# Kernel tuning notes

Measured on AMD Instinct MI355X. Metric: run time of the kernel, lower is better.

## Reference

```python
import jax, jax.numpy as jnp
import numpy as np

N = 50000
E = 800000
IN, HID, OUT = 256, 128, 128
H = 2


def gat_conv(x, edge_src, edge_dst, W, att_src, att_dst, bias, concat=True):
    # PyG GATConv: x' = W x, edge attention e = leaky_relu(a_s.x'_src + a_d.x'_dst),
    # softmax over incoming edges of each dst node, weighted scatter-add.
    n = x.shape[0]
    heads, ch = att_src.shape
    xl = (x @ W).reshape(n, heads, ch)                      # [N,H,C]
    a_src = jnp.sum(xl * att_src[None], axis=-1)            # [N,H]
    a_dst = jnp.sum(xl * att_dst[None], axis=-1)            # [N,H]
    e = a_src[edge_src] + a_dst[edge_dst]                   # [E,H]
    e = jax.nn.leaky_relu(e, negative_slope=0.2)
    # segment softmax over dst neighborhoods (self-loops guarantee non-empty)
    emax = jax.ops.segment_max(e, edge_dst, num_segments=n)
    ee = jnp.exp(e - emax[edge_dst])
    denom = jax.ops.segment_sum(ee, edge_dst, num_segments=n)
    alpha = ee / (denom[edge_dst] + 1e-16)                  # [E,H]
    msg = xl[edge_src] * alpha[:, :, None]                  # [E,H,C]
    out = jax.ops.segment_sum(msg, edge_dst, num_segments=n)  # [N,H,C]
    out = out.reshape(n, heads * ch) if concat else out.mean(axis=1)
    return out + bias


def setup_inputs() -> dict:
    key = jax.random.key(0)
    ks = jax.random.split(key, 12)
    x = jax.random.normal(ks[0], (N, IN), dtype=jnp.float32)
    edge_index = jax.random.randint(ks[1], (2, E), 0, N, dtype=jnp.int64)
    node_type = (jnp.arange(N, dtype=jnp.int64) % 3)
    agent_idx = jnp.arange(0, N, 3, dtype=jnp.int64)  # nodes with type 0
    # layer 0: in=256 -> out=128, heads=2, concat
    W0 = jax.random.normal(ks[2], (IN, H * HID), dtype=jnp.float32) / np.sqrt(IN)
    as0 = jax.random.normal(ks[3], (H, HID), dtype=jnp.float32) / np.sqrt(HID)
    ad0 = jax.random.normal(ks[4], (H, HID), dtype=jnp.float32) / np.sqrt(HID)
    b0 = jnp.zeros((H * HID,), dtype=jnp.float32)
    # layer 1: in=128*2 -> out=128, heads=2, concat (average_last=False)
    W1 = jax.random.normal(ks[5], (H * HID, H * OUT), dtype=jnp.float32) / np.sqrt(H * HID)
    as1 = jax.random.normal(ks[6], (H, OUT), dtype=jnp.float32) / np.sqrt(OUT)
    ad1 = jax.random.normal(ks[7], (H, OUT), dtype=jnp.float32) / np.sqrt(OUT)
    b1 = jnp.zeros((H * OUT,), dtype=jnp.float32)
    return {"x": x, "edge_index": edge_index, "node_type": node_type,
            "agent_idx": agent_idx, "W0": W0, "as0": as0, "ad0": ad0, "b0": b0,
            "W1": W1, "as1": as1, "ad1": ad1, "b1": b1}


def reference(x, edge_index, node_type, agent_idx, W0, as0, ad0, b0, W1, as1, ad1, b1):
    # add self loops (PyG GATConv default add_self_loops=True)
    loop = jnp.arange(N, dtype=edge_index.dtype)
    src = jnp.concatenate([edge_index[0], loop])
    dst = jnp.concatenate([edge_index[1], loop])
    final = []
    h = gat_conv(x, src, dst, W0, as0, ad0, b0, concat=True)
    h = jax.nn.sigmoid(h)
    final.append(h[agent_idx])  # full_receptive_field=True
    h = gat_conv(h, src, dst, W1, as1, ad1, b1, concat=True)
    h = jax.nn.sigmoid(h)
    final.append(h[agent_idx])
    return jnp.concatenate(final, axis=1)  # [n_agents, 128*2 + 128*2]
```

## Files before the change

kernel.cpp:

```cpp
#include <hip/hip_runtime.h>
#include <hip/hip_fp16.h>

typedef unsigned short u16;
typedef unsigned int   u32;
typedef unsigned char  u8;
typedef __attribute__((ext_vector_type(8))) short short8;
typedef __attribute__((ext_vector_type(8))) unsigned short ushort8v;
typedef __attribute__((ext_vector_type(4))) float f32x4;

#define TPB 256

#define GLDS16(g,l) __builtin_amdgcn_global_load_lds( \
    (const __attribute__((address_space(1))) void*)(g), \
    (__attribute__((address_space(3))) void*)(l), 16, 0, 0)

__device__ __forceinline__ float b2f(u16 u){ u32 x=((u32)u)<<16; return __uint_as_float(x); }
__device__ __forceinline__ u16 f2b(float f){ u32 x=__float_as_uint(f); u32 r=x+0x7FFFu+((x>>16)&1u); return (u16)(r>>16); }
__device__ __forceinline__ float lrelu(float x){ return x>0.f?x:0.2f*x; }
__device__ __forceinline__ float sigm(float x){ return 1.f/(1.f+__expf(-x)); }

__device__ __forceinline__ float4 ld4(const void* p, size_t i4, int isbf){
  if(isbf){
    ushort4 u=((const ushort4*)p)[i4];
    return make_float4(b2f(u.x),b2f(u.y),b2f(u.z),b2f(u.w));
  }
  return ((const float4*)p)[i4];
}
__device__ __forceinline__ float ld1(const void* p, size_t i, int isbf){
  return isbf ? b2f(((const u16*)p)[i]) : ((const float*)p)[i];
}

__global__ void k_detect(const u16* __restrict__ w, int* __restrict__ flag){
  __shared__ int s[256];
  int t=threadIdx.x, sane=0;
  for(int i=t;i<512;i+=256){
    u16 u=w[i]; u32 e=(u>>7)&0xFFu;
    if((e>=103u&&e<=143u)||((u&0x7FFFu)==0u)) sane++;
  }
  s[t]=sane; __syncthreads();
  for(int o=128;o;o>>=1){ if(t<o) s[t]+=s[t+o]; __syncthreads(); }
  if(t==0) flag[0]=(s[0]>=480)?1:0;
}

__global__ __launch_bounds__(256) void k_x8(const void* __restrict__ X, u16* __restrict__ xb,
                                            int n8, const int* __restrict__ flag){
  int i=blockIdx.x*256+threadIdx.x; if(i>=n8) return;
  size_t e=(size_t)i*8;
  if(flag[0]){
    *(ushort8v*)(xb+e)=*(const ushort8v*)((const u16*)X+e);
  }else{
    const float4* fp=(const float4*)((const float*)X+e);
    float4 f0=fp[0], f1=fp[1];
    ushort8v o;
    o[0]=f2b(f0.x); o[1]=f2b(f0.y); o[2]=f2b(f0.z); o[3]=f2b(f0.w);
    o[4]=f2b(f1.x); o[5]=f2b(f1.y); o[6]=f2b(f1.z); o[7]=f2b(f1.w);
    *(ushort8v*)(xb+e)=o;
  }
}

__global__ void k_deg(const int* __restrict__ dst, int E, int N, int* __restrict__ deg){
  int e=blockIdx.x*blockDim.x+threadIdx.x; if(e>=E+N) return;
  int d=(e<E)?dst[e]:(e-E);
  d=min(max(d,0),N-1);
  atomicAdd(&deg[d],1);
}

__global__ void k_scan(const int* __restrict__ deg, int* __restrict__ rs,
                       int* __restrict__ counter, int n,
                       const int* __restrict__ aidx, int* __restrict__ ainv, int na){
  __shared__ int tmp[TPB];
  __shared__ int base;
  int i=blockIdx.x*TPB+threadIdx.x;
  if(i<na){ int a=aidx[i]; if(a>=0&&a<n) ainv[a]=i; }
  int v=(i<n)?deg[i]:0;
  tmp[threadIdx.x]=v; __syncthreads();
  for(int off=1;off<TPB;off<<=1){
    int t=(threadIdx.x>=off)?tmp[threadIdx.x-off]:0;
    __syncthreads();
    tmp[threadIdx.x]+=t;
    __syncthreads();
  }
  if(threadIdx.x==TPB-1) base=atomicAdd(counter,tmp[TPB-1]);
  __syncthreads();
  if(i<n) rs[i]=base+tmp[threadIdx.x]-v;
}

__global__ void k_fill(const int* __restrict__ src, const int* __restrict__ dst, int E, int N,
                       const int* __restrict__ rs, int* __restrict__ fill, int* __restrict__ col){
  int e=blockIdx.x*blockDim.x+threadIdx.x; if(e>=E+N) return;
  int d,s;
  if(e<E){ d=dst[e]; s=src[e]; } else { d=e-E; s=e-E; }
  d=min(max(d,0),N-1); s=min(max(s,0),N-1);
  int p=rs[d]+atomicAdd(&fill[d],1);
  col[p]=s;
}

__global__ __launch_bounds__(256) void k_trans(const void* __restrict__ Wa, u16* __restrict__ WTa,
                                               const void* __restrict__ Wb, u16* __restrict__ WTb,
                                               const int* __restrict__ flag){
  __shared__ float s[64][65];
  const void* W = blockIdx.z ? Wb : Wa;
  u16* WT = blockIdx.z ? WTb : WTa;
  const int isbf=flag[0];
  int tx=threadIdx.x&63, ty=threadIdx.x>>6;
  int k0=blockIdx.x*64, n0=blockIdx.y*64;
  #pragma unroll
  for(int i=0;i<64;i+=4)
    s[ty+i][tx]=ld1(W,(size_t)(k0+ty+i)*256+n0+tx,isbf);
  __syncthreads();
  #pragma unroll
  for(int i=0;i<64;i+=4)
    WT[(size_t)(n0+ty+i)*256+k0+tx]=f2b(s[tx][ty+i]);
}

__global__ __launch_bounds__(256) void k_gemm(const u16* __restrict__ A, const u16* __restrict__ BT,
                                              u16* __restrict__ C, int M){
  __shared__ short As[128*32];
  __shared__ short Bs[128*32];
  const int t=threadIdx.x;
  const int lane=t&63, wv=t>>6;
  const int wm=wv>>1, wn=wv&1;
  const int m15=lane&15, kg=lane>>4;
  const int gm0=blockIdx.x*128, n0=blockIdx.y*128;
  int r0=wv*32+(lane>>2), r1=r0+16;
  int slot=lane&3;
  int kq0=slot^((r0>>1)&3), kq1=slot^((r1>>1)&3);
  int ga0=gm0+r0; ga0=ga0<M?ga0:M-1;
  int ga1=gm0+r1; ga1=ga1<M?ga1:M-1;
  const u16* ap0=A+(size_t)ga0*256+kq0*8;
  const u16* ap1=A+(size_t)ga1*256+kq1*8;
  const u16* bp0=BT+(size_t)(n0+r0)*256+kq0*8;
  const u16* bp1=BT+(size_t)(n0+r1)*256+kq1*8;
  short* al0=As+(wv*32)*32;
  short* al1=As+(wv*32+16)*32;
  short* bl0=Bs+(wv*32)*32;
  short* bl1=Bs+(wv*32+16)*32;
  f32x4 acc[4][4]={};
  for(int k0=0;k0<256;k0+=32){
    GLDS16(ap0+k0,al0); GLDS16(ap1+k0,al1);
    GLDS16(bp0+k0,bl0); GLDS16(bp1+k0,bl1);
    __syncthreads();
    short8 af[4], bf[4];
    #pragma unroll
    for(int mi=0;mi<4;++mi){
      int row=wm*64+mi*16+m15;
      af[mi]=*(const short8*)&As[row*32+((kg^((row>>1)&3)))*8];
    }
    #pragma unroll
    for(int ni=0;ni<4;++ni){
      int row=wn*64+ni*16+m15;
      bf[ni]=*(const short8*)&Bs[row*32+((kg^((row>>1)&3)))*8];
    }
    #pragma unroll
    for(int mi=0;mi<4;++mi)
      #pragma unroll
      for(int ni=0;ni<4;++ni)
        acc[mi][ni]=__builtin_amdgcn_mfma_f32_16x16x32_bf16(af[mi],bf[ni],acc[mi][ni],0,0,0);
    __syncthreads();
  }
  #pragma unroll
  for(int mi=0;mi<4;++mi){
    #pragma unroll
    for(int r=0;r<4;++r){
      int grow=gm0+wm*64+mi*16+kg*4+r;
      if(grow<M){
        #pragma unroll
        for(int ni=0;ni<4;++ni){
          int gcol=n0+wn*64+ni*16+m15;
          C[(size_t)grow*256+gcol]=f2b(acc[mi][ni][r]);
        }
      }
    }
  }
}

__global__ __launch_bounds__(256) void k_att(const u16* __restrict__ xl, const void* __restrict__ as_,
                                             const void* __restrict__ ad_, float4* __restrict__ asv,
                                             float2* __restrict__ adv, u8* __restrict__ xl8,
                                             int n, const int* __restrict__ flag){
  const int isbf=flag[0];
  int w=(blockIdx.x*256+threadIdx.x)>>6;
  int lane=threadIdx.x&63;
  if(w>=n) return;
  int ch=lane*4;
  ushort4 u=*(const ushort4*)(xl+(size_t)w*256+ch);
  float4 s=ld4(as_,ch>>2,isbf);
  float4 d=ld4(ad_,ch>>2,isbf);
  float x0=b2f(u.x),x1=b2f(u.y),x2=b2f(u.z),x3=b2f(u.w);
  float m=fmaxf(fmaxf(fabsf(x0),fabsf(x1)),fmaxf(fabsf(x2),fabsf(x3)));
  for(int off=32;off;off>>=1) m=fmaxf(m,__shfl_xor(m,off));
  float mm=fmaxf(m,1e-20f);
  float scale=mm*(1.f/127.f);
  float rsc=127.f/mm;
  int q0=(int)rintf(fmaf(x0,rsc,128.f));
  int q1=(int)rintf(fmaf(x1,rsc,128.f));
  int q2=(int)rintf(fmaf(x2,rsc,128.f));
  int q3=(int)rintf(fmaf(x3,rsc,128.f));
  u32 pack=(u32)q0|((u32)q1<<8)|((u32)q2<<16)|((u32)q3<<24);
  ((u32*)(xl8+(size_t)w*256))[lane]=pack;
  float ps=x0*s.x+x1*s.y+x2*s.z+x3*s.w;
  float pd=x0*d.x+x1*d.y+x2*d.z+x3*d.w;
  for(int off=16;off;off>>=1){ ps+=__shfl_xor(ps,off); pd+=__shfl_xor(pd,off); }
  float ps1=__shfl(ps,32), pd1=__shfl(pd,32);
  if(lane==0){
    asv[w]=make_float4(ps,ps1,scale,0.f);
    adv[w]=make_float2(pd,pd1);
  }
}

__global__ __launch_bounds__(256) void k_alpha(const int* __restrict__ rs, const int* __restrict__ deg,
    const int* __restrict__ col, const float4* __restrict__ asv, const float2* __restrict__ adv,
    int2* __restrict__ ew, float2* __restrict__ rden, int n){
  int w=(blockIdx.x*256+threadIdx.x)>>6;
  int lane=threadIdx.x&63;
  if(w>=n) return;
  int s0=rs[w], cnt=deg[w];
  float2 ad=adv[w];
  float sum0=0.f, sum1=0.f;
  for(int base=0;base<cnt;base+=64){
    int j=base+lane;
    if(j<cnt){
      int sv=col[s0+j];
      float4 a=asv[sv];
      float e0=fminf(lrelu(a.x+ad.x),11.f);
      float e1=fminf(lrelu(a.y+ad.y),11.f);
      float w0=__expf(e0), w1=__expf(e1);
      sum0+=w0; sum1+=w1;
      __half2 p=__floats2half2_rn(w0*a.z,w1*a.z);
      ew[s0+j]=make_int2(sv,*(int*)&p);
    }
  }
  for(int off=32;off;off>>=1){ sum0+=__shfl_xor(sum0,off); sum1+=__shfl_xor(sum1,off); }
  if(lane==0) rden[w]=make_float2(1.f/(sum0+1e-16f),1.f/(sum1+1e-16f));
}

__global__ __launch_bounds__(256) void k_agg(const int* __restrict__ rs, const int* __restrict__ deg,
    const int2* __restrict__ ew, const float2* __restrict__ rden,
    const u8* __restrict__ xl8, const void* __restrict__ bias,
    u16* __restrict__ hout, void* __restrict__ out, int ostride, int ocol,
    const int* __restrict__ ainv, int n, const int* __restrict__ flag){
  const int isbf=flag[0];
  int w=(blockIdx.x*blockDim.x+threadIdx.x)>>5;
  int sl=threadIdx.x&31;
  if(w>=n) return;
  int s0=rs[w], cnt=deg[w];
  int ch=sl*8, h=sl>>4;
  float acc[8]={};
  float sumw=0.f;
  for(int j=0;j<cnt;j+=4){
    int2 e[4];
    #pragma unroll
    for(int u=0;u<4;++u){
      int idx=j+u; idx=idx<cnt?idx:cnt-1;
      e[u]=ew[s0+idx];
    }
    uint2 rv[4];
    #pragma unroll
    for(int u=0;u<4;++u)
      rv[u]=*(const uint2*)(xl8+(size_t)e[u].x*256+ch);
    #pragma unroll
    for(int u=0;u<4;++u){
      __half2 p=*(__half2*)&e[u].y;
      float wb=__half2float(h?__high2half(p):__low2half(p));
      wb=(j+u<cnt)?wb:0.f;
      u32 a=rv[u].x, b=rv[u].y;
      acc[0]=fmaf(wb,(float)( a     &255u),acc[0]);
      acc[1]=fmaf(wb,(float)((a>> 8)&255u),acc[1]);
      acc[2]=fmaf(wb,(float)((a>>16)&255u),acc[2]);
      acc[3]=fmaf(wb,(float)( a>>24      ),acc[3]);
      acc[4]=fmaf(wb,(float)( b     &255u),acc[4]);
      acc[5]=fmaf(wb,(float)((b>> 8)&255u),acc[5]);
      acc[6]=fmaf(wb,(float)((b>>16)&255u),acc[6]);
      acc[7]=fmaf(wb,(float)( b>>24      ),acc[7]);
      sumw+=wb;
    }
  }
  float2 rd=rden[w];
  float rh=h?rd.y:rd.x;
  float4 b0=ld4(bias,ch>>2,isbf);
  float4 b1=ld4(bias,(ch>>2)+1,isbf);
  float c=128.f*sumw;
  float r[8];
  r[0]=sigm((acc[0]-c)*rh+b0.x); r[1]=sigm((acc[1]-c)*rh+b0.y);
  r[2]=sigm((acc[2]-c)*rh+b0.z); r[3]=sigm((acc[3]-c)*rh+b0.w);
  r[4]=sigm((acc[4]-c)*rh+b1.x); r[5]=sigm((acc[5]-c)*rh+b1.y);
  r[6]=sigm((acc[6]-c)*rh+b1.z); r[7]=sigm((acc[7]-c)*rh+b1.w);
  ushort8v ov;
  #pragma unroll
  for(int q=0;q<8;++q) ov[q]=f2b(r[q]);
  if(hout) *(ushort8v*)(hout+(size_t)w*256+ch)=ov;
  int ar=ainv[w];
  if(ar>=0){
    size_t o=(size_t)ar*ostride+ocol+ch;
    if(isbf){
      *(ushort8v*)((u16*)out+o)=ov;
    }else{
      *(float4*)((float*)out+o)  =make_float4(r[0],r[1],r[2],r[3]);
      *(float4*)((float*)out+o+4)=make_float4(r[4],r[5],r[6],r[7]);
    }
  }
}

extern "C" void kernel_launch(void* const* d_in, const int* in_sizes, int n_in,
                              void* d_out, int out_size, void* d_ws, size_t ws_size,
                              hipStream_t stream) {
  const void* x   = d_in[0];
  const int*  ei  = (const int*)d_in[1];
  const int*  aidx= (const int*)d_in[3];
  const void* W0  = d_in[4];
  const void* as0 = d_in[5];
  const void* ad0 = d_in[6];
  const void* b0  = d_in[7];
  const void* W1  = d_in[8];
  const void* as1 = d_in[9];
  const void* ad1 = d_in[10];
  const void* b1  = d_in[11];

  const int N  = in_sizes[0]/256;
  const int E  = in_sizes[1]/2;
  const int na = in_sizes[3];
  const int Et = E+N;

  char* ws=(char*)d_ws; size_t off=0;
  auto alloc=[&](size_t bytes)->void*{ void* p=ws+off; off+=(bytes+255)&~(size_t)255; return p; };
  int*   flg =(int*) alloc(256);
  u16*   xl  =(u16*) alloc((size_t)N*256*2);
  u16*   h1  =(u16*) alloc((size_t)N*256*2);
  u8*    xl8 =(u8*)  alloc((size_t)N*256);
  u16*   WT0 =(u16*) alloc((size_t)256*256*2);
  u16*   WT1 =(u16*) alloc((size_t)256*256*2);
  float4* asv=(float4*)alloc((size_t)N*16);
  float2* adv=(float2*)alloc((size_t)N*8);
  char*  zbase=ws+off;
  int*   deg =(int*) alloc((size_t)N*4);
  int*   fill=(int*) alloc((size_t)N*4);
  int*   ctr =(int*) alloc(256);
  size_t zlen=(ws+off)-zbase;
  int*   rstp=(int*) alloc((size_t)N*4);
  int*   ainv=(int*) alloc((size_t)N*4);
  int*   col =(int*) alloc((size_t)Et*4);
  int2*  ew  =(int2*)alloc((size_t)Et*8);
  float2* rdn=(float2*)alloc((size_t)N*8);

  u16* xb = h1;

  const int* esrc=ei;
  const int* edst=ei+E;

  hipMemsetAsync(zbase,0,zlen,stream);
  hipMemsetAsync(ainv,0xFF,(size_t)N*4,stream);

  k_detect<<<1,256,0,stream>>>((const u16*)W0,flg);
  k_deg  <<<(Et+255)/256,256,0,stream>>>(edst,E,N,deg);
  k_scan <<<(N+TPB-1)/TPB,TPB,0,stream>>>(deg,rstp,ctr,N,aidx,ainv,na);
  k_fill <<<(Et+255)/256,256,0,stream>>>(esrc,edst,E,N,rstp,fill,col);
  k_trans<<<dim3(4,4,2),256,0,stream>>>(W0,WT0,W1,WT1,flg);
  k_x8   <<<(N*32+255)/256,256,0,stream>>>(x,xb,N*32,flg);

  dim3 gg((N+127)/128,2);
  k_gemm <<<gg,256,0,stream>>>(xb,WT0,xl,N);
  k_att  <<<(N+3)/4,256,0,stream>>>(xl,as0,ad0,asv,adv,xl8,N,flg);
  k_alpha<<<(N+3)/4,256,0,stream>>>(rstp,deg,col,asv,adv,ew,rdn,N);
  k_agg  <<<(N+7)/8,256,0,stream>>>(rstp,deg,ew,rdn,xl8,b0,h1,d_out,512,0,ainv,N,flg);
  k_gemm <<<gg,256,0,stream>>>(h1,WT1,xl,N);
  k_att  <<<(N+3)/4,256,0,stream>>>(xl,as1,ad1,asv,adv,xl8,N,flg);
  k_alpha<<<(N+3)/4,256,0,stream>>>(rstp,deg,col,asv,adv,ew,rdn,N);
  k_agg  <<<(N+7)/8,256,0,stream>>>(rstp,deg,ew,rdn,xl8,b1,(u16*)nullptr,d_out,512,256,ainv,N,flg);
}
```

Baseline: 386.0 us.

## Merge setup kernels, widen GEMM K-tile to 64, unroll aggregation by 8

Folds the dtype-detect kernel and the ainv memset into k_deg, and merges the weight transpose and input conversion into one k_prep launch, cutting launch count. The GEMM now stages 64-wide K tiles with an 8-way XOR swizzle, halving barrier iterations at the cost of more LDS. The aggregation loop gathers 8 neighbours per iteration instead of 4 to expose more memory-level parallelism, which raises register pressure. There is a possible race: k_deg block 0 writes the flag while other blocks run, but the flag is only read by later kernels, so this is fine.

```diff
diff --git a/kernel.cpp b/kernel.cpp
--- a/kernel.cpp
+++ b/kernel.cpp
@@ -30,37 +30,23 @@
   return isbf ? b2f(((const u16*)p)[i]) : ((const float*)p)[i];
 }
 
-__global__ void k_detect(const u16* __restrict__ w, int* __restrict__ flag){
-  __shared__ int s[256];
-  int t=threadIdx.x, sane=0;
-  for(int i=t;i<512;i+=256){
-    u16 u=w[i]; u32 e=(u>>7)&0xFFu;
-    if((e>=103u&&e<=143u)||((u&0x7FFFu)==0u)) sane++;
-  }
-  s[t]=sane; __syncthreads();
-  for(int o=128;o;o>>=1){ if(t<o) s[t]+=s[t+o]; __syncthreads(); }
-  if(t==0) flag[0]=(s[0]>=480)?1:0;
-}
-
-__global__ __launch_bounds__(256) void k_x8(const void* __restrict__ X, u16* __restrict__ xb,
-                                            int n8, const int* __restrict__ flag){
-  int i=blockIdx.x*256+threadIdx.x; if(i>=n8) return;
-  size_t e=(size_t)i*8;
-  if(flag[0]){
-    *(ushort8v*)(xb+e)=*(const ushort8v*)((const u16*)X+e);
-  }else{
-    const float4* fp=(const float4*)((const float*)X+e);
-    float4 f0=fp[0], f1=fp[1];
-    ushort8v o;
-    o[0]=f2b(f0.x); o[1]=f2b(f0.y); o[2]=f2b(f0.z); o[3]=f2b(f0.w);
-    o[4]=f2b(f1.x); o[5]=f2b(f1.y); o[6]=f2b(f1.z); o[7]=f2b(f1.w);
-    *(ushort8v*)(xb+e)=o;
-  }
-}
-
-__global__ void k_deg(const int* __restrict__ dst, int E, int N, int* __restrict__ deg){
-  int e=blockIdx.x*blockDim.x+threadIdx.x; if(e>=E+N) return;
-  int d=(e<E)?dst[e]:(e-E);
+__global__ void k_deg(const int* __restrict__ dst, int E, int N, int* __restrict__ deg,
+                      int* __restrict__ ainv, const u16* __restrict__ w0, int* __restrict__ flag){
+  int gid=blockIdx.x*blockDim.x+threadIdx.x;
+  if(blockIdx.x==0){
+    __shared__ int s[256];
+    int t=threadIdx.x, sane=0;
+    for(int i=t;i<512;i+=256){
+      u16 u=w0[i]; u32 e=(u>>7)&0xFFu;
+      if((e>=103u&&e<=143u)||((u&0x7FFFu)==0u)) sane++;
+    }
+    s[t]=sane; __syncthreads();
+    for(int o=128;o;o>>=1){ if(t<o) s[t]+=s[t+o]; __syncthreads(); }
+    if(t==0) flag[0]=(s[0]>=480)?1:0;
+  }
+  if(gid<N) ainv[gid]=-1;
+  if(gid>=E+N) return;
+  int d=(gid<E)?dst[gid]:(gid-E);
   d=min(max(d,0),N-1);
   atomicAdd(&deg[d],1);
 }
@@ -95,67 +81,84 @@
   col[p]=s;
 }
 
-__global__ __launch_bounds__(256) void k_trans(const void* __restrict__ Wa, u16* __restrict__ WTa,
-                                               const void* __restrict__ Wb, u16* __restrict__ WTb,
-                                               const int* __restrict__ flag){
-  __shared__ float s[64][65];
-  const void* W = blockIdx.z ? Wb : Wa;
-  u16* WT = blockIdx.z ? WTb : WTa;
+__global__ __launch_bounds__(256) void k_prep(const void* __restrict__ Wa, u16* __restrict__ WTa,
+                                              const void* __restrict__ Wb, u16* __restrict__ WTb,
+                                              const void* __restrict__ X, u16* __restrict__ xb,
+                                              int n8, const int* __restrict__ flag){
   const int isbf=flag[0];
-  int tx=threadIdx.x&63, ty=threadIdx.x>>6;
-  int k0=blockIdx.x*64, n0=blockIdx.y*64;
-  #pragma unroll
-  for(int i=0;i<64;i+=4)
-    s[ty+i][tx]=ld1(W,(size_t)(k0+ty+i)*256+n0+tx,isbf);
-  __syncthreads();
-  #pragma unroll
-  for(int i=0;i<64;i+=4)
-    WT[(size_t)(n0+ty+i)*256+k0+tx]=f2b(s[tx][ty+i]);
+  int bid=blockIdx.x;
+  if(bid<32){
+    __shared__ float s[64][65];
+    int z=bid>>4, y=(bid>>2)&3, xb_=bid&3;
+    const void* W = z ? Wb : Wa;
+    u16* WT = z ? WTb : WTa;
+    int tx=threadIdx.x&63, ty=threadIdx.x>>6;
+    int k0=xb_*64, n0=y*64;
+    #pragma unroll
+    for(int i=0;i<64;i+=4)
+      s[ty+i][tx]=ld1(W,(size_t)(k0+ty+i)*256+n0+tx,isbf);
+    __syncthreads();
+    #pragma unroll
+    for(int i=0;i<64;i+=4)
+      WT[(size_t)(n0+ty+i)*256+k0+tx]=f2b(s[tx][ty+i]);
+    return;
+  }
+  int i=(bid-32)*256+threadIdx.x; if(i>=n8) return;
+  size_t e=(size_t)i*8;
+  if(isbf){
+    *(ushort8v*)(xb+e)=*(const ushort8v*)((const u16*)X+e);
+  }else{
+    const float4* fp=(const float4*)((const float*)X+e);
+    float4 f0=fp[0], f1=fp[1];
+    ushort8v o;
+    o[0]=f2b(f0.x); o[1]=f2b(f0.y); o[2]=f2b(f0.z); o[3]=f2b(f0.w);
+    o[4]=f2b(f1.x); o[5]=f2b(f1.y); o[6]=f2b(f1.z); o[7]=f2b(f1.w);
+    *(ushort8v*)(xb+e)=o;
+  }
 }
 
 __global__ __launch_bounds__(256) void k_gemm(const u16* __restrict__ A, const u16* __restrict__ BT,
                                               u16* __restrict__ C, int M){
-  __shared__ short As[128*32];
-  __shared__ short Bs[128*32];
+  __shared__ short As[128*64];
+  __shared__ short Bs[128*64];
   const int t=threadIdx.x;
   const int lane=t&63, wv=t>>6;
   const int wm=wv>>1, wn=wv&1;
   const int m15=lane&15, kg=lane>>4;
   const int gm0=blockIdx.x*128, n0=blockIdx.y*128;
-  int r0=wv*32+(lane>>2), r1=r0+16;
-  int slot=lane&3;
-  int kq0=slot^((r0>>1)&3), kq1=slot^((r1>>1)&3);
-  int ga0=gm0+r0; ga0=ga0<M?ga0:M-1;
-  int ga1=gm0+r1; ga1=ga1<M?ga1:M-1;
-  const u16* ap0=A+(size_t)ga0*256+kq0*8;
-  const u16* ap1=A+(size_t)ga1*256+kq1*8;
-  const u16* bp0=BT+(size_t)(n0+r0)*256+kq0*8;
-  const u16* bp1=BT+(size_t)(n0+r1)*256+kq1*8;
-  short* al0=As+(wv*32)*32;
-  short* al1=As+(wv*32+16)*32;
-  short* bl0=Bs+(wv*32)*32;
-  short* bl1=Bs+(wv*32+16)*32;
+  const int sr=lane>>3, slot=lane&7;
   f32x4 acc[4][4]={};
-  for(int k0=0;k0<256;k0+=32){
-    GLDS16(ap0+k0,al0); GLDS16(ap1+k0,al1);
-    GLDS16(bp0+k0,bl0); GLDS16(bp1+k0,bl1);
-    __syncthreads();
-    short8 af[4], bf[4];
-    #pragma unroll
-    for(int mi=0;mi<4;++mi){
-      int row=wm*64+mi*16+m15;
-      af[mi]=*(const short8*)&As[row*32+((kg^((row>>1)&3)))*8];
-    }
-    #pragma unroll
-    for(int ni=0;ni<4;++ni){
-      int row=wn*64+ni*16+m15;
-      bf[ni]=*(const short8*)&Bs[row*32+((kg^((row>>1)&3)))*8];
-    }
-    #pragma unroll
-    for(int mi=0;mi<4;++mi)
+  for(int k0=0;k0<256;k0+=64){
+    #pragma unroll
+    for(int i=0;i<4;++i){
+      int r=wv*32+i*8+sr;
+      int kq=slot^(r&7);
+      int ga=gm0+r; ga=ga<M?ga:M-1;
+      GLDS16(A+(size_t)ga*256+k0+kq*8, As+(wv*32+i*8)*64);
+      GLDS16(BT+(size_t)(n0+r)*256+k0+kq*8, Bs+(wv*32+i*8)*64);
+    }
+    __syncthreads();
+    #pragma unroll
+    for(int s=0;s<2;++s){
+      short8 af[4], bf[4];
       #pragma unroll
-      for(int ni=0;ni<4;++ni)
-        acc[mi][ni]=__builtin_amdgcn_mfma_f32_16x16x32_bf16(af[mi],bf[ni],acc[mi][ni],0,0,0);
+      for(int mi=0;mi<4;++mi){
+        int row=wm*64+mi*16+m15;
+        int sl=(s*4+kg)^(row&7);
+        af[mi]=*(const short8*)&As[row*64+sl*8];
+      }
+      #pragma unroll
+      for(int ni=0;ni<4;++ni){
+        int row=wn*64+ni*16+m15;
+        int sl=(s*4+kg)^(row&7);
+        bf[ni]=*(const short8*)&Bs[row*64+sl*8];
+      }
+      #pragma unroll
+      for(int mi=0;mi<4;++mi)
+        #pragma unroll
+        for(int ni=0;ni<4;++ni)
+          acc[mi][ni]=__builtin_amdgcn_mfma_f32_16x16x32_bf16(af[mi],bf[ni],acc[mi][ni],0,0,0);
+    }
     __syncthreads();
   }
   #pragma unroll
@@ -247,19 +250,19 @@
   int ch=sl*8, h=sl>>4;
   float acc[8]={};
   float sumw=0.f;
-  for(int j=0;j<cnt;j+=4){
-    int2 e[4];
-    #pragma unroll
-    for(int u=0;u<4;++u){
+  for(int j=0;j<cnt;j+=8){
+    int2 e[8];
+    #pragma unroll
+    for(int u=0;u<8;++u){
       int idx=j+u; idx=idx<cnt?idx:cnt-1;
       e[u]=ew[s0+idx];
     }
-    uint2 rv[4];
-    #pragma unroll
-    for(int u=0;u<4;++u)
+    uint2 rv[8];
+    #pragma unroll
+    for(int u=0;u<8;++u)
       rv[u]=*(const uint2*)(xl8+(size_t)e[u].x*256+ch);
     #pragma unroll
-    for(int u=0;u<4;++u){
+    for(int u=0;u<8;++u){
       __half2 p=*(__half2*)&e[u].y;
       float wb=__half2float(h?__high2half(p):__low2half(p));
       wb=(j+u<cnt)?wb:0.f;
@@ -348,14 +351,11 @@
   const int* edst=ei+E;
 
   hipMemsetAsync(zbase,0,zlen,stream);
-  hipMemsetAsync(ainv,0xFF,(size_t)N*4,stream);
-
-  k_detect<<<1,256,0,stream>>>((const u16*)W0,flg);
-  k_deg  <<<(Et+255)/256,256,0,stream>>>(edst,E,N,deg);
+
+  k_deg  <<<(Et+255)/256,256,0,stream>>>(edst,E,N,deg,ainv,(const u16*)W0,flg);
   k_scan <<<(N+TPB-1)/TPB,TPB,0,stream>>>(deg,rstp,ctr,N,aidx,ainv,na);
   k_fill <<<(Et+255)/256,256,0,stream>>>(esrc,edst,E,N,rstp,fill,col);
-  k_trans<<<dim3(4,4,2),256,0,stream>>>(W0,WT0,W1,WT1,flg);
-  k_x8   <<<(N*32+255)/256,256,0,stream>>>(x,xb,N*32,flg);
+  k_prep <<<32+(N*32+255)/256,256,0,stream>>>(W0,WT0,W1,WT1,x,xb,N*32,flg);
 
   dim3 gg((N+127)/128,2);
   k_gemm <<<gg,256,0,stream>>>(xb,WT0,xl,N);
```

Result: no change. 381.0 us (-1.3%).
